# Kernel optimization log

Hardware: AMD Instinct MI355X
Metric: run time of the kernel (lower is better)

Reference implementation:

```python
import jax, jax.numpy as jnp
import numpy as np

N_NODES = 100000
D_FEAT = 128
N_EDGES = 1600000


def setup_inputs() -> dict:
    key = jax.random.key(0)
    k1, k2, k3 = jax.random.split(key, 3)
    node_tensor = jax.random.normal(k1, (N_NODES, D_FEAT), dtype=jnp.float32)
    edge_src = jax.random.randint(k2, (N_EDGES,), 0, N_NODES, dtype=jnp.int64)
    edge_dst = jax.random.randint(k3, (N_EDGES,), 0, N_NODES, dtype=jnp.int64)
    return {"node_tensor": node_tensor, "edge_src": edge_src, "edge_dst": edge_dst}


def reference(node_tensor, edge_src, edge_dst):
    # Depth-1 neighbourhood traversal: for each node, neighbourhood = {self} U {src of incoming edges}.
    # Mean reducer over the neighbourhood features, then concat onto node features (dim=1),
    # mirroring NodeGraphNeighbourhood.forward with include_self=True.
    n = node_tensor.shape[0]
    gathered = node_tensor[edge_src]                      # [E, D] irregular gather
    neigh_sum = jax.ops.segment_sum(gathered, edge_dst, num_segments=n)   # [N, D]
    deg = jax.ops.segment_sum(jnp.ones(edge_dst.shape[0], dtype=node_tensor.dtype),
                              edge_dst, num_segments=n)   # [N]
    reduced = (neigh_sum + node_tensor) / (deg + 1.0)[:, None]            # mean incl. self
    return jnp.concatenate((node_tensor, reduced), axis=1)               # [N, 2D]
```

## Files before the change

### kernel.cpp

```cpp
#include <hip/hip_runtime.h>

#define DFEAT 128
#define NBK_SHIFT 6
#define BNODES 64
#define SLOT 1536
#define CAP SLOT
#define CHUNK 4096
#define NBMAX 1600

typedef float v2f __attribute__((ext_vector_type(2)));


struct SmemScatter {
    int lcnt[NBMAX];
    int ldelta[NBMAX];
    int part[512];
    unsigned spair[CHUNK];
    unsigned short sbkt[CHUNK];
};

__global__ void ngn_zero_kernel(int* __restrict__ gcur, int nb) {
    int t = blockIdx.x * blockDim.x + threadIdx.x;
    if (t < nb) gcur[t] = 0;
}

__device__ __forceinline__ void convert_item(const float4* __restrict__ node4,
                                             uint2* __restrict__ nf,
                                             float4* __restrict__ out4, int t) {
    float4 a = node4[2 * t];
    float4 b = node4[2 * t + 1];
    unsigned lo = 0, hi = 0;
    lo = __builtin_amdgcn_cvt_pk_fp8_f32(a.x, a.y, lo, false);
    lo = __builtin_amdgcn_cvt_pk_fp8_f32(a.z, a.w, lo, true);
    hi = __builtin_amdgcn_cvt_pk_fp8_f32(b.x, b.y, hi, false);
    hi = __builtin_amdgcn_cvt_pk_fp8_f32(b.z, b.w, hi, true);
    nf[t] = make_uint2(lo, hi);
    int n = t >> 4;
    int j = t & 15;
    size_t orow = (size_t)n * 64;
    out4[orow + 2 * j] = a;
    out4[orow + 2 * j + 1] = b;
}

__device__ void scatter_chunk(SmemScatter& sm, const int4* __restrict__ src4,
                              const int4* __restrict__ dst4, int* __restrict__ gcur,
                              unsigned* __restrict__ pairbuf, int chunk,
                              int n_quads, int n_edges, int nb) {
    int tid = threadIdx.x;
    for (int i = tid; i < nb; i += 512) sm.lcnt[i] = 0;
    __syncthreads();

    int e0 = chunk * CHUNK;
    int e1 = min(e0 + CHUNK, n_edges);
    int q0 = e0 >> 2;
    int q1 = min(q0 + CHUNK / 4, n_quads);
    int ccnt = e1 - e0;

    for (int q = q0 + tid; q < q1; q += 512) {
        int4 d = dst4[q];
        int base = q * 4;
        if (base + 3 < n_edges) {
            atomicAdd(&sm.lcnt[d.x >> NBK_SHIFT], 1);
            atomicAdd(&sm.lcnt[d.y >> NBK_SHIFT], 1);
            atomicAdd(&sm.lcnt[d.z >> NBK_SHIFT], 1);
            atomicAdd(&sm.lcnt[d.w >> NBK_SHIFT], 1);
        } else {
            const int* dd = (const int*)&d;
            for (int k = 0; k < 4 && base + k < n_edges; ++k)
                atomicAdd(&sm.lcnt[dd[k] >> NBK_SHIFT], 1);
        }
    }
    __syncthreads();

    {
        int t4 = tid * 4;
        int s = 0;
#pragma unroll
        for (int k = 0; k < 4; ++k) {
            int idx = t4 + k;
            if (idx < nb) s += sm.lcnt[idx];
        }
        sm.part[tid] = s;
        __syncthreads();
        for (int d = 1; d < 512; d <<= 1) {
            int v = sm.part[tid];
            int a = (tid >= d) ? sm.part[tid - d] : 0;
            __syncthreads();
            sm.part[tid] = v + a;
            __syncthreads();
        }
        int run = sm.part[tid] - s;
#pragma unroll
        for (int k = 0; k < 4; ++k) {
            int idx = t4 + k;
            if (idx < nb) {
                int c = sm.lcnt[idx];
                int lofs = run;
                run += c;
                int lbase = c ? atomicAdd(&gcur[idx], c) : 0;
                sm.lcnt[idx] = lofs;
                sm.ldelta[idx] = lbase - lofs;
            }
        }
    }
    __syncthreads();

    for (int q = q0 + tid; q < q1; q += 512) {
        int4 s = src4[q];
        int4 d = dst4[q];
        int base = q * 4;
        const int* ss = (const int*)&s;
        const int* dd = (const int*)&d;
        int kmax = (base + 3 < n_edges) ? 4 : (n_edges - base);
        for (int k = 0; k < kmax; ++k) {
            int dv = dd[k];
            int b = dv >> NBK_SHIFT;
            int pos = atomicAdd(&sm.lcnt[b], 1);
            sm.spair[pos] = ((unsigned)(dv & (BNODES - 1)) << 17) | (unsigned)ss[k];
            sm.sbkt[pos] = (unsigned short)b;
        }
    }
    __syncthreads();

    for (int i = tid; i < ccnt; i += 512) {
        int b = sm.sbkt[i];
        int fill = sm.ldelta[b] + i;
        if (fill < SLOT) pairbuf[(size_t)b * SLOT + fill] = sm.spair[i];
    }
}

__global__ void __launch_bounds__(512)
ngn_prep_kernel(const float4* __restrict__ node4,
                const int4* __restrict__ src4, const int4* __restrict__ dst4,
                uint2* __restrict__ nf, unsigned* __restrict__ pairbuf,
                int* __restrict__ gcur, float4* __restrict__ out4,
                int n_edges, int nb, int nchunks, int total_cv) {
    __shared__ SmemScatter sm;
    int bid = blockIdx.x;
    int n_quads = (n_edges + 3) >> 2;
    if (bid < nchunks) {
        scatter_chunk(sm, src4, dst4, gcur, pairbuf, bid, n_quads, n_edges, nb);
    } else {
        int t = (bid - nchunks) * 512 + threadIdx.x;
        if (t < total_cv) convert_item(node4, nf, out4, t);
    }
}

__device__ __forceinline__ void acc8_fp8(uint2 w, float& a0, float& a1, float& a2, float& a3,
                                         float& a4, float& a5, float& a6, float& a7) {
    v2f f0 = __builtin_amdgcn_cvt_pk_f32_fp8(w.x, false);
    v2f f1 = __builtin_amdgcn_cvt_pk_f32_fp8(w.x, true);
    v2f f2 = __builtin_amdgcn_cvt_pk_f32_fp8(w.y, false);
    v2f f3 = __builtin_amdgcn_cvt_pk_f32_fp8(w.y, true);
    a0 += f0.x; a1 += f0.y; a2 += f1.x; a3 += f1.y;
    a4 += f2.x; a5 += f2.y; a6 += f3.x; a7 += f3.y;
}

__global__ void __launch_bounds__(512)
ngn_passB_kernel(const float4* __restrict__ node4,
                 const uint2* __restrict__ nf2,
                 const unsigned* __restrict__ pairbuf,
                 const int* __restrict__ gcur,
                 float4* __restrict__ out4, int n_nodes) {
    __shared__ int lhist[BNODES];
    __shared__ int loff[BNODES];
    __shared__ int lcur[BNODES];
    __shared__ unsigned srt[CAP];

    int b = blockIdx.x;
    int node0 = b << NBK_SHIFT;
    int nnodes = min(BNODES, n_nodes - node0);
    int cnt = min(gcur[b], SLOT);
    const unsigned* pb = pairbuf + (size_t)b * SLOT;
    int tid = threadIdx.x;
    int wave = tid >> 6, lane = tid & 63;
    int q = lane >> 4;
    int fl = lane & 15;

    if (tid < BNODES) lhist[tid] = 0;
    __syncthreads();
    for (int i = tid; i < cnt; i += 512) atomicAdd(&lhist[pb[i] >> 17], 1);
    __syncthreads();
    if (wave == 0) {
        int v = lhist[lane];
        int p = v;
        for (int d = 1; d < 64; d <<= 1) {
            int t2 = __shfl_up(p, d);
            if (lane >= d) p += t2;
        }
        loff[lane] = p - v;
        lcur[lane] = p - v;
    }
    __syncthreads();
    for (int i = tid; i < cnt; i += 512) {
        unsigned p = pb[i];
        int pos = atomicAdd(&lcur[p >> 17], 1);
        srt[pos] = p & 0x1FFFFu;
    }
    __syncthreads();

    for (int l = wave; l < nnodes; l += 8) {
        int o0 = loff[l];
        int deg = lhist[l];
        int n = node0 + l;
        float a0 = 0.f, a1 = 0.f, a2 = 0.f, a3 = 0.f;
        float a4 = 0.f, a5 = 0.f, a6 = 0.f, a7 = 0.f;
        int i = 0;
        for (; i + 16 <= deg; i += 16) {
            int s0 = srt[o0 + i + q];
            int s1 = srt[o0 + i + 4 + q];
            int s2 = srt[o0 + i + 8 + q];
            int s3 = srt[o0 + i + 12 + q];
            uint2 w0 = nf2[(size_t)s0 * 16 + fl];
            uint2 w1 = nf2[(size_t)s1 * 16 + fl];
            uint2 w2 = nf2[(size_t)s2 * 16 + fl];
            uint2 w3 = nf2[(size_t)s3 * 16 + fl];
            acc8_fp8(w0, a0, a1, a2, a3, a4, a5, a6, a7);
            acc8_fp8(w1, a0, a1, a2, a3, a4, a5, a6, a7);
            acc8_fp8(w2, a0, a1, a2, a3, a4, a5, a6, a7);
            acc8_fp8(w3, a0, a1, a2, a3, a4, a5, a6, a7);
        }
        for (; i + 4 <= deg; i += 4) {
            int s0 = srt[o0 + i + q];
            uint2 w0 = nf2[(size_t)s0 * 16 + fl];
            acc8_fp8(w0, a0, a1, a2, a3, a4, a5, a6, a7);
        }
        int rem = deg - i;
        if (q < rem) {
            int s0 = srt[o0 + i + q];
            uint2 w0 = nf2[(size_t)s0 * 16 + fl];
            acc8_fp8(w0, a0, a1, a2, a3, a4, a5, a6, a7);
        }
        a0 += __shfl_xor(a0, 16); a1 += __shfl_xor(a1, 16);
        a2 += __shfl_xor(a2, 16); a3 += __shfl_xor(a3, 16);
        a4 += __shfl_xor(a4, 16); a5 += __shfl_xor(a5, 16);
        a6 += __shfl_xor(a6, 16); a7 += __shfl_xor(a7, 16);
        a0 += __shfl_xor(a0, 32); a1 += __shfl_xor(a1, 32);
        a2 += __shfl_xor(a2, 32); a3 += __shfl_xor(a3, 32);
        a4 += __shfl_xor(a4, 32); a5 += __shfl_xor(a5, 32);
        a6 += __shfl_xor(a6, 32); a7 += __shfl_xor(a7, 32);
        if (q == 0) {
            float4 s0 = node4[(size_t)n * 32 + 2 * fl];
            float4 s1 = node4[(size_t)n * 32 + 2 * fl + 1];
            float inv = 1.0f / (float)(deg + 1);
            float4 r0, r1;
            r0.x = (a0 + s0.x) * inv; r0.y = (a1 + s0.y) * inv;
            r0.z = (a2 + s0.z) * inv; r0.w = (a3 + s0.w) * inv;
            r1.x = (a4 + s1.x) * inv; r1.y = (a5 + s1.y) * inv;
            r1.z = (a6 + s1.z) * inv; r1.w = (a7 + s1.w) * inv;
            out4[(size_t)n * 64 + 32 + 2 * fl] = r0;
            out4[(size_t)n * 64 + 32 + 2 * fl + 1] = r1;
        }
    }
}

extern "C" void kernel_launch(void* const* d_in, const int* in_sizes, int n_in,
                              void* d_out, int out_size, void* d_ws, size_t ws_size,
                              hipStream_t stream) {
    const float4* node4 = (const float4*)d_in[0];
    const int4* src4 = (const int4*)d_in[1];
    const int4* dst4 = (const int4*)d_in[2];
    float4* out4 = (float4*)d_out;

    int n_nodes = in_sizes[0] / DFEAT;
    int n_edges = in_sizes[1];
    int nb = (n_nodes + BNODES - 1) >> NBK_SHIFT;
    int nchunks = (n_edges + CHUNK - 1) / CHUNK;
    int total_cv = n_nodes * (DFEAT / 8);

    uint2* nf = (uint2*)d_ws;
    unsigned* pairbuf = (unsigned*)(nf + (size_t)n_nodes * (DFEAT / 8));
    int* gcur = (int*)(pairbuf + (size_t)nb * SLOT);

    ngn_zero_kernel<<<(nb + 511) / 512, 512, 0, stream>>>(gcur, nb);

    int cv_blocks = (total_cv + 511) / 512;
    ngn_prep_kernel<<<nchunks + cv_blocks, 512, 0, stream>>>(
        node4, src4, dst4, nf, pairbuf, gcur, out4, n_edges, nb, nchunks, total_cv);

    ngn_passB_kernel<<<nb, 512, 0, stream>>>(node4, nf, pairbuf, gcur, out4, n_nodes);
}
```

Baseline: 110.4 us.

## Replace global atomic bucket slots with per-chunk offset table and gather-side merge

The scatter stage no longer reserves space in per-bucket global slots with atomics. Each chunk now writes its locally bucket-sorted pairs contiguously and records a per-chunk row of bucket offsets. The aggregation kernel scans all chunks' offset rows for its bucket, prefix-sums the counts and gathers the pairs into shared memory. This removes the zero kernel and the global atomics. In exchange, each aggregation block must read about 391 offset pairs and make many small, scattered serial reads, which may cost more than it saves.

```diff
diff --git a/kernel.cpp b/kernel.cpp
--- a/kernel.cpp
+++ b/kernel.cpp
@@ -3,8 +3,7 @@
 #define DFEAT 128
 #define NBK_SHIFT 6
 #define BNODES 64
-#define SLOT 1536
-#define CAP SLOT
+#define CAP 1536
 #define CHUNK 4096
 #define NBMAX 1600
 
@@ -13,16 +12,9 @@
 
 struct SmemScatter {
     int lcnt[NBMAX];
-    int ldelta[NBMAX];
     int part[512];
     unsigned spair[CHUNK];
-    unsigned short sbkt[CHUNK];
 };
-
-__global__ void ngn_zero_kernel(int* __restrict__ gcur, int nb) {
-    int t = blockIdx.x * blockDim.x + threadIdx.x;
-    if (t < nb) gcur[t] = 0;
-}
 
 __device__ __forceinline__ void convert_item(const float4* __restrict__ node4,
                                              uint2* __restrict__ nf,
@@ -43,9 +35,9 @@
 }
 
 __device__ void scatter_chunk(SmemScatter& sm, const int4* __restrict__ src4,
-                              const int4* __restrict__ dst4, int* __restrict__ gcur,
-                              unsigned* __restrict__ pairbuf, int chunk,
-                              int n_quads, int n_edges, int nb) {
+                              const int4* __restrict__ dst4,
+                              unsigned* __restrict__ pairbuf, int* __restrict__ glofs,
+                              int chunk, int n_quads, int n_edges, int nb) {
     int tid = threadIdx.x;
     for (int i = tid; i < nb; i += 512) sm.lcnt[i] = 0;
     __syncthreads();
@@ -72,6 +64,7 @@
     }
     __syncthreads();
 
+    int* lrow = glofs + (size_t)chunk * (nb + 1);
     {
         int t4 = tid * 4;
         int s = 0;
@@ -95,13 +88,12 @@
             int idx = t4 + k;
             if (idx < nb) {
                 int c = sm.lcnt[idx];
-                int lofs = run;
+                lrow[idx] = run;
+                sm.lcnt[idx] = run;
                 run += c;
-                int lbase = c ? atomicAdd(&gcur[idx], c) : 0;
-                sm.lcnt[idx] = lofs;
-                sm.ldelta[idx] = lbase - lofs;
             }
         }
+        if (tid == 0) lrow[nb] = ccnt;
     }
     __syncthreads();
 
@@ -117,29 +109,25 @@
             int b = dv >> NBK_SHIFT;
             int pos = atomicAdd(&sm.lcnt[b], 1);
             sm.spair[pos] = ((unsigned)(dv & (BNODES - 1)) << 17) | (unsigned)ss[k];
-            sm.sbkt[pos] = (unsigned short)b;
-        }
-    }
-    __syncthreads();
-
-    for (int i = tid; i < ccnt; i += 512) {
-        int b = sm.sbkt[i];
-        int fill = sm.ldelta[b] + i;
-        if (fill < SLOT) pairbuf[(size_t)b * SLOT + fill] = sm.spair[i];
-    }
+        }
+    }
+    __syncthreads();
+
+    unsigned* pout = pairbuf + (size_t)chunk * CHUNK;
+    for (int i = tid; i < ccnt; i += 512) pout[i] = sm.spair[i];
 }
 
 __global__ void __launch_bounds__(512)
 ngn_prep_kernel(const float4* __restrict__ node4,
                 const int4* __restrict__ src4, const int4* __restrict__ dst4,
                 uint2* __restrict__ nf, unsigned* __restrict__ pairbuf,
-                int* __restrict__ gcur, float4* __restrict__ out4,
+                int* __restrict__ glofs, float4* __restrict__ out4,
                 int n_edges, int nb, int nchunks, int total_cv) {
     __shared__ SmemScatter sm;
     int bid = blockIdx.x;
     int n_quads = (n_edges + 3) >> 2;
     if (bid < nchunks) {
-        scatter_chunk(sm, src4, dst4, gcur, pairbuf, bid, n_quads, n_edges, nb);
+        scatter_chunk(sm, src4, dst4, pairbuf, glofs, bid, n_quads, n_edges, nb);
     } else {
         int t = (bid - nchunks) * 512 + threadIdx.x;
         if (t < total_cv) convert_item(node4, nf, out4, t);
@@ -160,26 +148,54 @@
 ngn_passB_kernel(const float4* __restrict__ node4,
                  const uint2* __restrict__ nf2,
                  const unsigned* __restrict__ pairbuf,
-                 const int* __restrict__ gcur,
-                 float4* __restrict__ out4, int n_nodes) {
+                 const int* __restrict__ glofs,
+                 float4* __restrict__ out4, int n_nodes, int nchunks, int nb) {
     __shared__ int lhist[BNODES];
     __shared__ int loff[BNODES];
     __shared__ int lcur[BNODES];
+    __shared__ int part[512];
+    __shared__ unsigned stage[CAP];
     __shared__ unsigned srt[CAP];
 
     int b = blockIdx.x;
     int node0 = b << NBK_SHIFT;
     int nnodes = min(BNODES, n_nodes - node0);
-    int cnt = min(gcur[b], SLOT);
-    const unsigned* pb = pairbuf + (size_t)b * SLOT;
     int tid = threadIdx.x;
     int wave = tid >> 6, lane = tid & 63;
     int q = lane >> 4;
     int fl = lane & 15;
 
+    int tot = 0;
+    for (int c = tid; c < nchunks; c += 512) {
+        const int* lrow = glofs + (size_t)c * (nb + 1);
+        tot += lrow[b + 1] - lrow[b];
+    }
+    part[tid] = tot;
+    __syncthreads();
+    for (int d = 1; d < 512; d <<= 1) {
+        int v = part[tid];
+        int a = (tid >= d) ? part[tid - d] : 0;
+        __syncthreads();
+        part[tid] = v + a;
+        __syncthreads();
+    }
+    int base = part[tid] - tot;
+    int cnt = min(part[511], CAP);
+    int pos = base;
+    for (int c = tid; c < nchunks; c += 512) {
+        const int* lrow = glofs + (size_t)c * (nb + 1);
+        int s0 = lrow[b], s1 = lrow[b + 1];
+        const unsigned* pin = pairbuf + (size_t)c * CHUNK;
+        for (int j = s0; j < s1; ++j) {
+            if (pos < CAP) stage[pos] = pin[j];
+            ++pos;
+        }
+    }
+    __syncthreads();
+
     if (tid < BNODES) lhist[tid] = 0;
     __syncthreads();
-    for (int i = tid; i < cnt; i += 512) atomicAdd(&lhist[pb[i] >> 17], 1);
+    for (int i = tid; i < cnt; i += 512) atomicAdd(&lhist[stage[i] >> 17], 1);
     __syncthreads();
     if (wave == 0) {
         int v = lhist[lane];
@@ -193,9 +209,9 @@
     }
     __syncthreads();
     for (int i = tid; i < cnt; i += 512) {
-        unsigned p = pb[i];
-        int pos = atomicAdd(&lcur[p >> 17], 1);
-        srt[pos] = p & 0x1FFFFu;
+        unsigned p = stage[i];
+        int pp = atomicAdd(&lcur[p >> 17], 1);
+        srt[pp] = p & 0x1FFFFu;
     }
     __syncthreads();
 
@@ -270,13 +286,12 @@
 
     uint2* nf = (uint2*)d_ws;
     unsigned* pairbuf = (unsigned*)(nf + (size_t)n_nodes * (DFEAT / 8));
-    int* gcur = (int*)(pairbuf + (size_t)nb * SLOT);
-
-    ngn_zero_kernel<<<(nb + 511) / 512, 512, 0, stream>>>(gcur, nb);
+    int* glofs = (int*)(pairbuf + (size_t)nchunks * CHUNK);
 
     int cv_blocks = (total_cv + 511) / 512;
     ngn_prep_kernel<<<nchunks + cv_blocks, 512, 0, stream>>>(
-        node4, src4, dst4, nf, pairbuf, gcur, out4, n_edges, nb, nchunks, total_cv);
-
-    ngn_passB_kernel<<<nb, 512, 0, stream>>>(node4, nf, pairbuf, gcur, out4, n_nodes);
-}
+        node4, src4, dst4, nf, pairbuf, glofs, out4, n_edges, nb, nchunks, total_cv);
+
+    ngn_passB_kernel<<<nb, 512, 0, stream>>>(node4, nf, pairbuf, glofs, out4,
+                                             n_nodes, nchunks, nb);
+}
```

New measurement: 105.5 us. 4.4% less time.
